# Kernel optimization log

Hardware: AMD Instinct MI355X
Metric: run time of the kernel (lower is better)

## Reference

```python
import jax, jax.numpy as jnp
import numpy as np

B, S, D, H, T = 64, 512, 768, 384, 22  # batch, seq, bert dim, lstm hidden, tagset+2


def setup_inputs() -> dict:
    key = jax.random.key(0)
    ks = jax.random.split(key, 14)
    hidden_states = jax.random.normal(ks[0], (B, S, D), jnp.float32)
    # strictly increasing wordpiece start offsets, -1 padded (per-sample variable length)
    nw = np.array([S // 2 - (b % 16) * 4 for b in range(B)])  # number of valid start ids
    sid = -np.ones((B, S), np.int64)
    msk = np.zeros((B, S), np.int64)
    for b in range(B):
        sid[b, : nw[b]] = 1 + 2 * np.arange(nw[b])  # max = 2*nw-1 <= S-1
        msk[b, : nw[b] + 1] = 1  # word-level mask: nw+1 words incl. CLS slot
    start_ids = jnp.asarray(sid)
    masks = jnp.asarray(msk)
    sc = 0.05
    h0 = jax.random.normal(ks[1], (2, B, H), jnp.float32)
    c0 = jax.random.normal(ks[2], (2, B, H), jnp.float32)
    W_ih_f = jax.random.normal(ks[3], (4 * H, D), jnp.float32) * sc
    W_hh_f = jax.random.normal(ks[4], (4 * H, H), jnp.float32) * sc
    b_ih_f = jax.random.normal(ks[5], (4 * H,), jnp.float32) * sc
    b_hh_f = jax.random.normal(ks[6], (4 * H,), jnp.float32) * sc
    W_ih_b = jax.random.normal(ks[7], (4 * H, D), jnp.float32) * sc
    W_hh_b = jax.random.normal(ks[8], (4 * H, H), jnp.float32) * sc
    b_ih_b = jax.random.normal(ks[9], (4 * H,), jnp.float32) * sc
    b_hh_b = jax.random.normal(ks[10], (4 * H,), jnp.float32) * sc
    W_lin = jax.random.normal(ks[11], (T, 2 * H), jnp.float32) * sc
    b_lin = jax.random.normal(ks[12], (T,), jnp.float32) * sc
    return {"hidden_states": hidden_states, "h0": h0, "c0": c0,
            "W_ih_f": W_ih_f, "W_hh_f": W_hh_f, "b_ih_f": b_ih_f, "b_hh_f": b_hh_f,
            "W_ih_b": W_ih_b, "W_hh_b": W_hh_b, "b_ih_b": b_ih_b, "b_hh_b": b_hh_b,
            "W_lin": W_lin, "b_lin": b_lin, "start_ids": start_ids, "masks": masks}


def _lstm_dir(x, h0, c0, Wih, Whh, bih, bhh, reverse):
    # x: [B,S,D]; torch gate order i,f,g,o
    xg = jnp.einsum('bsd,gd->bsg', x, Wih) + bih + bhh  # [B,S,4H]
    xs = jnp.swapaxes(xg, 0, 1)  # [S,B,4H]
    if reverse:
        xs = xs[::-1]

    def step(carry, xt):
        h, c = carry
        g = xt + h @ Whh.T
        i, f, gg, o = jnp.split(g, 4, axis=-1)
        c = jax.nn.sigmoid(f) * c + jax.nn.sigmoid(i) * jnp.tanh(gg)
        h = jax.nn.sigmoid(o) * jnp.tanh(c)
        return (h, c), h

    _, hs = jax.lax.scan(step, (h0, c0), xs)
    if reverse:
        hs = hs[::-1]
    return jnp.swapaxes(hs, 0, 1)  # [B,S,H]


def _align(hidden_states, start_ids, masks):
    # word t embedding: t==0 -> token 0 (CLS); 1<=t<n -> token start_ids[t]-1
    # (last wordpiece of word t); t==n -> token start_ids[n-1]; else zero-pad.
    Bb, Ss, _ = hidden_states.shape
    t = jnp.arange(Ss)[None, :]
    valid = start_ids >= 0
    n = valid.sum(-1)  # [B] number of valid start ids
    last_sid = jnp.take_along_axis(start_ids, (n - 1)[:, None], axis=1)  # [B,1]
    idx = jnp.where(t == 0, 0,
          jnp.where(t < n[:, None], start_ids - 1,
          jnp.where(t == n[:, None], last_sid, 0)))
    idx = jnp.clip(idx, 0, Ss - 1)
    gathered = jnp.take_along_axis(hidden_states, idx[:, :, None], axis=1)
    sent_len = masks.sum(-1)  # word-level lengths (second loop in torch code)
    keep = (t < sent_len[:, None])[:, :, None]
    return jnp.where(keep, gathered, 0.0)


def reference(hidden_states, h0, c0, W_ih_f, W_hh_f, b_ih_f, b_hh_f,
              W_ih_b, W_hh_b, b_ih_b, b_hh_b, W_lin, b_lin, start_ids, masks):
    embeds = _align(hidden_states, start_ids, masks)  # q=1,k=0 => wordpiece-only
    hf = _lstm_dir(embeds, h0[0], c0[0], W_ih_f, W_hh_f, b_ih_f, b_hh_f, False)
    hb = _lstm_dir(embeds, h0[1], c0[1], W_ih_b, W_hh_b, b_ih_b, b_hh_b, True)
    lstm_out = jnp.concatenate([hf, hb], axis=-1)  # [B,S,2H]
    # dropout1 is identity in eval mode
    feats = lstm_out @ W_lin.T + b_lin  # [B,S,T]
    return feats
```

## Files before the change

kernel.cpp:

```cpp
#include <hip/hip_runtime.h>

typedef unsigned short u16;
typedef unsigned int u32;
typedef unsigned long long u64;

typedef short bf16x8 __attribute__((ext_vector_type(8)));
typedef float f32x4 __attribute__((ext_vector_type(4)));
typedef u32 u32x4 __attribute__((ext_vector_type(4)));

#define NB 64
#define NS 512
#define ND 768
#define NH 384
#define NT_OUT 22
#define S2 272
#define NG 1536
#define MGEMM (NB*S2)
#define MAGIC 0x5A5AA5A5u
#define MAX_RETRY 1000000

__device__ __forceinline__ u16 f2b(float f) {
    u32 u = __float_as_uint(f);
    u32 r = (u + 0x7fffu + ((u >> 16) & 1u)) >> 16;
    return (u16)r;
}
__device__ __forceinline__ float b2f(u16 s) { return __uint_as_float(((u32)s) << 16); }

__device__ __forceinline__ float sigm(float x) {
    return __builtin_amdgcn_rcpf(1.f + __expf(-x));
}
__device__ __forceinline__ float tanh_(float x) {
    return 1.f - 2.f * __builtin_amdgcn_rcpf(1.f + __expf(2.f * x));
}

__device__ __forceinline__ void gl_lds16(const void* g, void* l) {
    __builtin_amdgcn_global_load_lds(
        (const __attribute__((address_space(1))) unsigned int*)g,
        (__attribute__((address_space(3))) unsigned int*)l, 16, 0, 0);
}

__device__ __forceinline__ u32 ld_sc0(const int* p) {
    u32 v;
    asm volatile("global_load_dword %0, %1, off sc0 nt\n\t"
                 "s_waitcnt vmcnt(0)"
                 : "=&v"(v) : "v"(p) : "memory");
    return v;
}
__device__ __forceinline__ void st_sc0(int* p, u32 v) {
    asm volatile("global_store_dword %0, %1, off sc0" :: "v"(p), "v"(v) : "memory");
}

__device__ __forceinline__ void ld6_fast_nw(const u32* p,
        u32x4& A, u32x4& B, u32x4& C, u32x4& D, u32x4& E, u32x4& F) {
    asm volatile(
        "global_load_dwordx4 %0, %6, off sc0 nt\n\t"
        "global_load_dwordx4 %1, %6, off offset:16 sc0 nt\n\t"
        "global_load_dwordx4 %2, %6, off offset:128 sc0 nt\n\t"
        "global_load_dwordx4 %3, %6, off offset:144 sc0 nt\n\t"
        "global_load_dwordx4 %4, %6, off offset:256 sc0 nt\n\t"
        "global_load_dwordx4 %5, %6, off offset:272 sc0 nt"
        : "=&v"(A), "=&v"(B), "=&v"(C), "=&v"(D), "=&v"(E), "=&v"(F)
        : "v"(p) : "memory");
}
__device__ __forceinline__ void ld6_fast_wt(const u32* p,
        u32x4& A, u32x4& B, u32x4& C, u32x4& D, u32x4& E, u32x4& F) {
    asm volatile(
        "global_load_dwordx4 %0, %6, off sc0 nt\n\t"
        "global_load_dwordx4 %1, %6, off offset:16 sc0 nt\n\t"
        "global_load_dwordx4 %2, %6, off offset:128 sc0 nt\n\t"
        "global_load_dwordx4 %3, %6, off offset:144 sc0 nt\n\t"
        "global_load_dwordx4 %4, %6, off offset:256 sc0 nt\n\t"
        "global_load_dwordx4 %5, %6, off offset:272 sc0 nt\n\t"
        "s_waitcnt vmcnt(0)"
        : "=&v"(A), "=&v"(B), "=&v"(C), "=&v"(D), "=&v"(E), "=&v"(F)
        : "v"(p) : "memory");
}
__device__ __forceinline__ void ld6_slow(const u32* p,
        u32x4& A, u32x4& B, u32x4& C, u32x4& D, u32x4& E, u32x4& F) {
    #pragma unroll
    for (int e = 0; e < 4; e++) {
        A[e] = __hip_atomic_load(p + e,      __ATOMIC_RELAXED, __HIP_MEMORY_SCOPE_AGENT);
        B[e] = __hip_atomic_load(p + 4 + e,  __ATOMIC_RELAXED, __HIP_MEMORY_SCOPE_AGENT);
        C[e] = __hip_atomic_load(p + 32 + e, __ATOMIC_RELAXED, __HIP_MEMORY_SCOPE_AGENT);
        D[e] = __hip_atomic_load(p + 36 + e, __ATOMIC_RELAXED, __HIP_MEMORY_SCOPE_AGENT);
        E[e] = __hip_atomic_load(p + 64 + e, __ATOMIC_RELAXED, __HIP_MEMORY_SCOPE_AGENT);
        F[e] = __hip_atomic_load(p + 68 + e, __ATOMIC_RELAXED, __HIP_MEMORY_SCOPE_AGENT);
    }
}
__device__ __forceinline__ void ld6_nw(bool fast, const u32* p,
        u32x4& A, u32x4& B, u32x4& C, u32x4& D, u32x4& E, u32x4& F) {
    if (fast) ld6_fast_nw(p, A, B, C, D, E, F);
    else      ld6_slow(p, A, B, C, D, E, F);
}
__device__ __forceinline__ void ld6_wt(bool fast, const u32* p,
        u32x4& A, u32x4& B, u32x4& C, u32x4& D, u32x4& E, u32x4& F) {
    if (fast) ld6_fast_wt(p, A, B, C, D, E, F);
    else      ld6_slow(p, A, B, C, D, E, F);
}
__device__ __forceinline__ void st8(bool fast, u32* p, u32x4 lo, u32x4 hi) {
    if (fast)
        asm volatile("global_store_dwordx4 %0, %1, off sc0\n\t"
                     "global_store_dwordx4 %0, %2, off offset:16 sc0"
                     :: "v"(p), "v"(lo), "v"(hi) : "memory");
    else {
        #pragma unroll
        for (int e = 0; e < 4; e++) {
            __hip_atomic_store(p + e,     lo[e], __ATOMIC_RELAXED, __HIP_MEMORY_SCOPE_AGENT);
            __hip_atomic_store(p + 4 + e, hi[e], __ATOMIC_RELAXED, __HIP_MEMORY_SCOPE_AGENT);
        }
    }
}
__device__ __forceinline__ void wait_vm6() {
    __builtin_amdgcn_sched_barrier(0);
    asm volatile("s_waitcnt vmcnt(6)" ::: "memory");
    __builtin_amdgcn_sched_barrier(0);
}
__device__ __forceinline__ void wait_vm0() {
    __builtin_amdgcn_sched_barrier(0);
    asm volatile("s_waitcnt vmcnt(0)" ::: "memory");
    __builtin_amdgcn_sched_barrier(0);
}
__device__ __forceinline__ void ldsbar() {
    asm volatile("s_waitcnt lgkmcnt(0)" ::: "memory");
    __builtin_amdgcn_s_barrier();
    __builtin_amdgcn_sched_barrier(0);
}

__device__ __forceinline__ u32 sum6(const u32x4& a, const u32x4& b, const u32x4& c,
                                    const u32x4& d, const u32x4& e, const u32x4& f) {
    u32 s = (a[0] & 0xffffu) + (a[1] & 0xffffu) + (a[2] & 0xffffu) + (a[3] & 0xffffu);
    s += (b[0] & 0xffffu) + (b[1] & 0xffffu) + (b[2] & 0xffffu) + (b[3] & 0xffffu);
    s += (c[0] & 0xffffu) + (c[1] & 0xffffu) + (c[2] & 0xffffu) + (c[3] & 0xffffu);
    s += (d[0] & 0xffffu) + (d[1] & 0xffffu) + (d[2] & 0xffffu) + (d[3] & 0xffffu);
    s += (e[0] & 0xffffu) + (e[1] & 0xffffu) + (e[2] & 0xffffu) + (e[3] & 0xffffu);
    s += (f[0] & 0xffffu) + (f[1] & 0xffffu) + (f[2] & 0xffffu) + (f[3] & 0xffffu);
    return s;
}
__device__ __forceinline__ bf16x8 packf(const u32x4& lo, const u32x4& hi) {
    union { u32 q[4]; bf16x8 v; } U;
    U.q[0] = __builtin_amdgcn_perm(lo[1], lo[0], 0x07060302u);
    U.q[1] = __builtin_amdgcn_perm(lo[3], lo[2], 0x07060302u);
    U.q[2] = __builtin_amdgcn_perm(hi[1], hi[0], 0x07060302u);
    U.q[3] = __builtin_amdgcn_perm(hi[3], hi[2], 0x07060302u);
    return U.v;
}

__global__ void k_prep(const float* __restrict__ hidden, const int* __restrict__ start_ids,
                       const int* __restrict__ masks, u16* __restrict__ embeds) {
    int b = blockIdx.x >> 2;
    int quarter = blockIdx.x & 3;
    int tid = threadIdx.x;
    __shared__ int red[256];
    int cn = 0, cm = 0;
    for (int s = tid; s < NS; s += 256) {
        cn += (start_ids[b * NS + s] >= 0) ? 1 : 0;
        cm += (masks[b * NS + s] != 0) ? 1 : 0;
    }
    red[tid] = cn + (cm << 16);
    __syncthreads();
    #pragma unroll
    for (int off = 128; off > 0; off >>= 1) {
        if (tid < off) red[tid] += red[tid + off];
        __syncthreads();
    }
    int n = red[0] & 0xffff;
    int slen = red[0] >> 16;
    n = min(max(n, 1), NS);
    int last = start_ids[b * NS + n - 1];
    for (int t = quarter * 68; t < quarter * 68 + 68; ++t) {
        int idx;
        if (t == 0) idx = 0;
        else if (t < n) idx = start_ids[b * NS + t] - 1;
        else if (t == n) idx = last;
        else idx = 0;
        idx = min(max(idx, 0), NS - 1);
        bool keep = t < slen;
        const float* src = hidden + ((size_t)b * NS + idx) * ND;
        u16* dst = embeds + ((size_t)b * S2 + t) * ND;
        if (tid < 192) {
            float4 v = keep ? *(const float4*)(src + tid * 4) : make_float4(0.f, 0.f, 0.f, 0.f);
            union { u16 u[4]; uint2 q; } pk;
            pk.u[0] = f2b(v.x); pk.u[1] = f2b(v.y); pk.u[2] = f2b(v.z); pk.u[3] = f2b(v.w);
            *(uint2*)(dst + tid * 4) = pk.q;
        }
    }
}

__global__ void k_weights(const float* __restrict__ wf, const float* __restrict__ wb,
                          const float* __restrict__ bihf, const float* __restrict__ bhhf,
                          const float* __restrict__ bihb, const float* __restrict__ bhhb,
                          const float* __restrict__ h0,
                          u16* __restrict__ wihcat, float* __restrict__ biascat,
                          u16* __restrict__ h0buf) {
    int i0 = blockIdx.x * blockDim.x + threadIdx.x;
    int NTH = gridDim.x * blockDim.x;
    for (size_t i = i0; i < (size_t)2 * NG * ND; i += NTH) {
        size_t nrow = i / ND, k = i - nrow * ND;
        float v = (nrow < NG) ? wf[nrow * ND + k] : wb[(nrow - NG) * ND + k];
        wihcat[i] = f2b(v);
    }
    for (int i = i0; i < 2 * NG; i += NTH)
        biascat[i] = (i < NG) ? bihf[i] + bhhf[i] : bihb[i - NG] + bhhb[i - NG];
    for (int i = i0; i < 2 * NB * NH; i += NTH) h0buf[i] = f2b(h0[i]);
}

__global__ void k_packwhh(const float* __restrict__ whhf, const float* __restrict__ whhb,
                          u16* __restrict__ pack) {
    int ft = blockIdx.x * 256 + threadIdx.x;
    if (ft >= 2 * 4 * 4 * 6 * 12 * 64) return;
    int lane = ft & 63;
    int grp = ft >> 6;
    int ks = grp % 12; grp /= 12;
    int nt = grp % 6;  grp /= 6;
    int w  = grp & 3;  grp >>= 2;
    int qc = grp & 3;
    int d  = grp >> 2;
    const float* W = d ? whhb : whhf;
    int col = w * NH + qc * 96 + nt * 16 + (lane & 15);
    int k0 = ks * 32 + (lane >> 4) * 8;
    u16* dst = pack + (size_t)ft * 8;
    #pragma unroll
    for (int e = 0; e < 8; e++) dst[e] = f2b(W[(size_t)col * NH + k0 + e]);
}

__launch_bounds__(256, 2)
__global__ void k_gemm(const u16* __restrict__ A, const u16* __restrict__ Bw,
                       const float* __restrict__ biascat, u16* __restrict__ xg) {
    __shared__ u16 As[128 * 32];
    __shared__ u16 Bs[128 * 32];
    int tid = threadIdx.x;
    int lane = tid & 63, wid = tid >> 6;
    int l15 = lane & 15, q4 = lane >> 4;
    int bn = blockIdx.x;
    int bm = blockIdx.y;
    int wm = (wid >> 1) * 64, wn = (wid & 1) * 64;
    f32x4 acc[4][4] = {};
    for (int k0 = 0; k0 < ND; k0 += 32) {
        #pragma unroll
        for (int j = 0; j < 2; j++) {
            int fl = tid + j * 256;
            int row = fl >> 2, cb = fl & 3;
            const u16* ga = A + (size_t)(bm * 128 + row) * ND + k0 + cb * 8;
            gl_lds16(ga, &As[(size_t)(wid * 64 + j * 256) * 8]);
            const u16* gb = Bw + (size_t)(bn * 128 + row) * ND + k0 + cb * 8;
            gl_lds16(gb, &Bs[(size_t)(wid * 64 + j * 256) * 8]);
        }
        __syncthreads();
        bf16x8 af[4], bf[4];
        #pragma unroll
        for (int mt = 0; mt < 4; mt++)
            af[mt] = *(const bf16x8*)&As[(wm + mt * 16 + l15) * 32 + q4 * 8];
        #pragma unroll
        for (int nt = 0; nt < 4; nt++)
            bf[nt] = *(const bf16x8*)&Bs[(wn + nt * 16 + l15) * 32 + q4 * 8];
        #pragma unroll
        for (int mt = 0; mt < 4; mt++)
            #pragma unroll
            for (int nt = 0; nt < 4; nt++)
                acc[mt][nt] = __builtin_amdgcn_mfma_f32_16x16x32_bf16(af[mt], bf[nt], acc[mt][nt], 0, 0, 0);
        __syncthreads();
    }
    #pragma unroll
    for (int nt = 0; nt < 4; nt++) {
        int gn = bn * 128 + wn + nt * 16 + l15;
        int d = gn >= NG ? 1 : 0;
        int col = gn - d * NG;
        float bias = biascat[gn];
        #pragma unroll
        for (int mt = 0; mt < 4; mt++) {
            #pragma unroll
            for (int r = 0; r < 4; r++) {
                int m = bm * 128 + wm + mt * 16 + q4 * 4 + r;
                int b = m / S2, t = m - b * S2;
                float v = acc[mt][nt][r] + bias;
                xg[((size_t)(d * NB + b) * S2 + t) * NG + col] = f2b(v);
            }
        }
    }
}

__launch_bounds__(256, 1)
__global__ void k_recur(const u16* __restrict__ whhpack, const u16* __restrict__ xg,
                        const float* __restrict__ biascat, const u16* __restrict__ h0buf,
                        const float* __restrict__ c0, u16* __restrict__ hout,
                        int* __restrict__ flags, u32* __restrict__ xch) {
    const int blk = blockIdx.x;
    const int qc = blk >> 3;
    const int cl = blk & 7;
    const int d = cl >> 2;
    const int g = cl & 3;
    const int tid = threadIdx.x, lane = tid & 63, w = tid >> 6;
    const int q4 = lane >> 4, l15 = lane & 15;

    __shared__ float preact[4][16 * 96];
    __shared__ u16 hlds[16 * 104];
    __shared__ int s_fast;

    bf16x8 bfr[6][12];
    #pragma unroll
    for (int nt = 0; nt < 6; nt++)
        #pragma unroll
        for (int j = 0; j < 12; j++) {
            int ksg = ((qc + (j / 3)) & 3) * 3 + (j % 3);
            bfr[nt][j] = *(const bf16x8*)(whhpack +
                ((size_t)((((d * 4 + qc) * 4 + w) * 6 + nt) * 12 + ksg) * 64 + lane) * 8);
        }

    const int bb = tid / 12;
    const int j0 = (tid % 12) * 8;
    float cre[8];
    if (tid < 192) {
        const float* cp = c0 + (size_t)(d * NB + g * 16 + bb) * NH + qc * 96 + j0;
        #pragma unroll
        for (int e = 0; e < 8; e++) cre[e] = cp[e];
    }
    float biasreg[6];
    #pragma unroll
    for (int nt = 0; nt < 6; nt++)
        biasreg[nt] = biascat[d * NG + w * NH + qc * 96 + nt * 16 + l15];

    if (tid == 0) {
        int* pzb = flags + cl * 64;
        int* pmb = flags + 2048 + cl * 64;
        st_sc0(pzb + qc * 16, MAGIC);
        u32 seen = 1u << qc;
        for (int spin = 0; spin < 512 && seen != 0xFu; ++spin) {
            #pragma unroll
            for (int r = 0; r < 4; ++r)
                if (!((seen >> r) & 1u) && ld_sc0(pzb + r * 16) == MAGIC) seen |= 1u << r;
            __builtin_amdgcn_s_sleep(2);
        }
        __hip_atomic_store(pmb + qc * 16, (int)(0x100u | seen),
                           __ATOMIC_RELAXED, __HIP_MEMORY_SCOPE_AGENT);
        u32 m = 0xFu;
        int spin2 = 0;
        #pragma unroll
        for (int r = 0; r < 4; ++r) {
            u32 v;
            do {
                v = (u32)__hip_atomic_load(pmb + r * 16, __ATOMIC_RELAXED,
                                           __HIP_MEMORY_SCOPE_AGENT);
            } while (!(v & 0x100u) && ++spin2 < MAX_RETRY);
            m &= v;
        }
        s_fast = ((m & 0xFu) == 0xFu && spin2 < MAX_RETRY) ? 1 : 0;
    }
    __syncthreads();
    const bool fast = (s_fast != 0);

    const u16* xgd = xg + (size_t)d * NB * S2 * NG;

    float ci[6][4];
    auto preload = [&](int it2) {
        int s2 = d ? (NS - 1 - it2) : it2;
        if (s2 < S2) {
            const u16* xrow = xgd + ((size_t)(g * 16) * S2 + s2) * NG + w * NH + qc * 96 + l15;
            #pragma unroll
            for (int nt = 0; nt < 6; nt++)
                #pragma unroll
                for (int r = 0; r < 4; r++)
                    ci[nt][r] = b2f(xrow[(size_t)(q4 * 4 + r) * S2 * NG + nt * 16]);
        } else {
            #pragma unroll
            for (int nt = 0; nt < 6; nt++)
                #pragma unroll
                for (int r = 0; r < 4; r++) ci[nt][r] = biasreg[nt];
        }
    };
    preload(0);

    #pragma unroll 1
    for (int it = 0; it < NS; ++it) {
        int s = d ? (NS - 1 - it) : it;
        f32x4 acc[6];

        if (it == 0) {
            bf16x8 af0[12];
            const u16* hp = h0buf + (size_t)(d * NB + g * 16) * NH;
            #pragma unroll
            for (int j = 0; j < 12; j++) {
                int ksg = ((qc + (j / 3)) & 3) * 3 + (j % 3);
                af0[j] = *(const bf16x8*)(hp + (size_t)l15 * NH + ksg * 32 + q4 * 8);
            }
            #pragma unroll
            for (int nt = 0; nt < 6; nt++) {
                acc[nt][0] = ci[nt][0]; acc[nt][1] = ci[nt][1];
                acc[nt][2] = ci[nt][2]; acc[nt][3] = ci[nt][3];
            }
            preload(1);
            #pragma unroll
            for (int j = 0; j < 12; j++)
                #pragma unroll
                for (int nt = 0; nt < 6; nt++)
                    acc[nt] = __builtin_amdgcn_mfma_f32_16x16x32_bf16(af0[j], bfr[nt][j], acc[nt], 0, 0, 0);
        } else {
            bf16x8 afo0 = *(const bf16x8*)&hlds[l15 * 104 + 0 * 32 + q4 * 8];
            bf16x8 afo1 = *(const bf16x8*)&hlds[l15 * 104 + 1 * 32 + q4 * 8];
            bf16x8 afo2 = *(const bf16x8*)&hlds[l15 * 104 + 2 * 32 + q4 * 8];
            const u32 T = (u32)it;
            const u32 want = T * 24u;
            u32* xrow = xch + (((size_t)(T & 3u) * 8 + cl) * 16 + l15) * 384 + q4 * 8;
            u32* pA = xrow + ((qc + 1) & 3) * 96;
            u32* pB = xrow + ((qc + 2) & 3) * 96;
            u32* pC = xrow + ((qc + 3) & 3) * 96;
            u32x4 a0, a1, a2, a3, a4, a5, b0, b1, b2, b3, b4, b5, e0, e1, e2, e3, e4, e5;
            ld6_nw(fast, pA, a0, a1, a2, a3, a4, a5);
            ld6_nw(fast, pB, b0, b1, b2, b3, b4, b5);
            #pragma unroll
            for (int nt = 0; nt < 6; nt++) {
                acc[nt][0] = ci[nt][0]; acc[nt][1] = ci[nt][1];
                acc[nt][2] = ci[nt][2]; acc[nt][3] = ci[nt][3];
            }
            #pragma unroll
            for (int nt = 0; nt < 6; nt++)
                acc[nt] = __builtin_amdgcn_mfma_f32_16x16x32_bf16(afo0, bfr[nt][0], acc[nt], 0, 0, 0);
            #pragma unroll
            for (int nt = 0; nt < 6; nt++)
                acc[nt] = __builtin_amdgcn_mfma_f32_16x16x32_bf16(afo1, bfr[nt][1], acc[nt], 0, 0, 0);
            #pragma unroll
            for (int nt = 0; nt < 6; nt++)
                acc[nt] = __builtin_amdgcn_mfma_f32_16x16x32_bf16(afo2, bfr[nt][2], acc[nt], 0, 0, 0);
            wait_vm6();
            int tries = 0;
            while (!__all(sum6(a0, a1, a2, a3, a4, a5) == want) && ++tries < MAX_RETRY)
                ld6_wt(fast, pA, a0, a1, a2, a3, a4, a5);
            bf16x8 afA0 = packf(a0, a1), afA1 = packf(a2, a3), afA2 = packf(a4, a5);
            ld6_nw(fast, pC, e0, e1, e2, e3, e4, e5);
            #pragma unroll
            for (int nt = 0; nt < 6; nt++)
                acc[nt] = __builtin_amdgcn_mfma_f32_16x16x32_bf16(afA0, bfr[nt][3], acc[nt], 0, 0, 0);
            #pragma unroll
            for (int nt = 0; nt < 6; nt++)
                acc[nt] = __builtin_amdgcn_mfma_f32_16x16x32_bf16(afA1, bfr[nt][4], acc[nt], 0, 0, 0);
            #pragma unroll
            for (int nt = 0; nt < 6; nt++)
                acc[nt] = __builtin_amdgcn_mfma_f32_16x16x32_bf16(afA2, bfr[nt][5], acc[nt], 0, 0, 0);
            wait_vm6();
            tries = 0;
            while (!__all(sum6(b0, b1, b2, b3, b4, b5) == want) && ++tries < MAX_RETRY)
                ld6_wt(fast, pB, b0, b1, b2, b3, b4, b5);
            bf16x8 afB0 = packf(b0, b1), afB1 = packf(b2, b3), afB2 = packf(b4, b5);
            #pragma unroll
            for (int nt = 0; nt < 6; nt++)
                acc[nt] = __builtin_amdgcn_mfma_f32_16x16x32_bf16(afB0, bfr[nt][6], acc[nt], 0, 0, 0);
            #pragma unroll
            for (int nt = 0; nt < 6; nt++)
                acc[nt] = __builtin_amdgcn_mfma_f32_16x16x32_bf16(afB1, bfr[nt][7], acc[nt], 0, 0, 0);
            #pragma unroll
            for (int nt = 0; nt < 6; nt++)
                acc[nt] = __builtin_amdgcn_mfma_f32_16x16x32_bf16(afB2, bfr[nt][8], acc[nt], 0, 0, 0);
            wait_vm0();
            tries = 0;
            while (!__all(sum6(e0, e1, e2, e3, e4, e5) == want) && ++tries < MAX_RETRY)
                ld6_wt(fast, pC, e0, e1, e2, e3, e4, e5);
            bf16x8 afC0 = packf(e0, e1), afC1 = packf(e2, e3), afC2 = packf(e4, e5);
            if (it + 1 < NS) preload(it + 1);
            #pragma unroll
            for (int nt = 0; nt < 6; nt++)
                acc[nt] = __builtin_amdgcn_mfma_f32_16x16x32_bf16(afC0, bfr[nt][9], acc[nt], 0, 0, 0);
            #pragma unroll
            for (int nt = 0; nt < 6; nt++)
                acc[nt] = __builtin_amdgcn_mfma_f32_16x16x32_bf16(afC1, bfr[nt][10], acc[nt], 0, 0, 0);
            #pragma unroll
            for (int nt = 0; nt < 6; nt++)
                acc[nt] = __builtin_amdgcn_mfma_f32_16x16x32_bf16(afC2, bfr[nt][11], acc[nt], 0, 0, 0);
        }

        #pragma unroll
        for (int nt = 0; nt < 6; nt++)
            #pragma unroll
            for (int r = 0; r < 4; r++)
                preact[w][(q4 * 4 + r) * 96 + nt * 16 + l15] = acc[nt][r];
        ldsbar();

        if (tid < 192) {
            int idx = bb * 96 + j0;
            u16* ho = hout + (((size_t)(d * NB + g * 16 + bb)) * NS + s) * NH + qc * 96 + j0;
            union { u16 u[8]; u32x4 v4; } pk;
            #pragma unroll
            for (int e = 0; e < 8; e++) {
                float gi = preact[0][idx + e], gf = preact[1][idx + e];
                float gg = preact[2][idx + e], go = preact[3][idx + e];
                float c = cre[e];
                float cn = sigm(gf) * c + sigm(gi) * tanh_(gg);
                float hn = sigm(go) * tanh_(cn);
                cre[e] = cn;
                pk.u[e] = f2b(hn);
            }
            u32 t2 = (u32)it + 1u;
            u32x4 lo, hi;
            lo[0] = ((u32)pk.u[0] << 16) | t2; lo[1] = ((u32)pk.u[1] << 16) | t2;
            lo[2] = ((u32)pk.u[2] << 16) | t2; lo[3] = ((u32)pk.u[3] << 16) | t2;
            hi[0] = ((u32)pk.u[4] << 16) | t2; hi[1] = ((u32)pk.u[5] << 16) | t2;
            hi[2] = ((u32)pk.u[6] << 16) | t2; hi[3] = ((u32)pk.u[7] << 16) | t2;
            u32* xp = xch + (((size_t)(t2 & 3u) * 8 + cl) * 16 + bb) * 384 + qc * 96 + j0;
            st8(fast, xp, lo, hi);
            *(u32x4*)ho = pk.v4;
            *(u32x4*)&hlds[bb * 104 + j0] = pk.v4;
        }
        wait_vm0();
        ldsbar();
    }
}

__global__ void k_final(const u16* __restrict__ hout, const float* __restrict__ wlin,
                        const float* __restrict__ blin, float* __restrict__ out) {
    int r = blockIdx.x * 256 + threadIdx.x;
    int b = r >> 9, t = r & 511;
    const u16* hf = hout + ((size_t)b * NS + t) * NH;
    const u16* hb = hout + ((size_t)(NB + b) * NS + t) * NH;
    float acc[NT_OUT];
    #pragma unroll
    for (int tt = 0; tt < NT_OUT; tt++) acc[tt] = blin[tt];
    #pragma unroll 1
    for (int half = 0; half < 2; half++) {
        const u16* hp = half ? hb : hf;
        #pragma unroll 1
        for (int k8 = 0; k8 < NH / 8; k8++) {
            uint4 pk = *(const uint4*)(hp + k8 * 8);
            float x[8];
            x[0] = __uint_as_float(pk.x << 16); x[1] = __uint_as_float(pk.x & 0xffff0000u);
            x[2] = __uint_as_float(pk.y << 16); x[3] = __uint_as_float(pk.y & 0xffff0000u);
            x[4] = __uint_as_float(pk.z << 16); x[5] = __uint_as_float(pk.z & 0xffff0000u);
            x[6] = __uint_as_float(pk.w << 16); x[7] = __uint_as_float(pk.w & 0xffff0000u);
            int kk = half * NH + k8 * 8;
            #pragma unroll
            for (int e = 0; e < 8; e++)
                #pragma unroll
                for (int tt = 0; tt < NT_OUT; tt++)
                    acc[tt] += x[e] * wlin[tt * (2 * NH) + kk + e];
        }
    }
    float* op = out + (size_t)r * NT_OUT;
    #pragma unroll
    for (int tt = 0; tt < NT_OUT; tt++) op[tt] = acc[tt];
}

extern "C" void kernel_launch(void* const* d_in, const int* in_sizes, int n_in,
                              void* d_out, int out_size, void* d_ws, size_t ws_size,
                              hipStream_t stream) {
    const float* hidden = (const float*)d_in[0];
    const float* h0     = (const float*)d_in[1];
    const float* c0     = (const float*)d_in[2];
    const float* Wihf   = (const float*)d_in[3];
    const float* Whhf   = (const float*)d_in[4];
    const float* bihf   = (const float*)d_in[5];
    const float* bhhf   = (const float*)d_in[6];
    const float* Wihb   = (const float*)d_in[7];
    const float* Whhb   = (const float*)d_in[8];
    const float* bihb   = (const float*)d_in[9];
    const float* bhhb   = (const float*)d_in[10];
    const float* Wlin   = (const float*)d_in[11];
    const float* blin   = (const float*)d_in[12];
    const int* start_ids = (const int*)d_in[13];
    const int* masks     = (const int*)d_in[14];
    float* out = (float*)d_out;

    char* ws = (char*)d_ws;
    size_t off = 0;
    auto alloc = [&](size_t bytes) { void* p = ws + off; off += (bytes + 255) & ~(size_t)255; return p; };
    u16* embeds   = (u16*)alloc((size_t)MGEMM * ND * 2);
    u16* wihcat   = (u16*)alloc((size_t)2 * NG * ND * 2);
    float* biascat = (float*)alloc((size_t)2 * NG * 4);
    u16* whhpack  = (u16*)alloc((size_t)2 * NG * NH * 2);
    u16* h0buf    = (u16*)alloc((size_t)2 * NB * NH * 2);
    u16* xg       = (u16*)alloc((size_t)2 * NB * S2 * NG * 2);
    u16* hout     = (u16*)alloc((size_t)2 * NB * NS * NH * 2);
    int* flags    = (int*)alloc((size_t)8 * NS * 4);
    u32* xch      = (u32*)alloc((size_t)4 * 8 * 16 * 384 * 4);

    (void)hipMemsetAsync(flags, 0, (size_t)8 * NS * 4, stream);
    (void)hipMemsetAsync(xch, 0, (size_t)4 * 8 * 16 * 384 * 4, stream);
    k_prep<<<256, 256, 0, stream>>>(hidden, start_ids, masks, embeds);
    k_weights<<<512, 256, 0, stream>>>(Wihf, Wihb, bihf, bhhf, bihb, bhhb, h0,
                                       wihcat, biascat, h0buf);
    k_packwhh<<<576, 256, 0, stream>>>(Whhf, Whhb, whhpack);
    dim3 ggrid(2 * NG / 128, MGEMM / 128);
    k_gemm<<<ggrid, 256, 0, stream>>>(embeds, wihcat, biascat, xg);
    k_recur<<<32, 256, 0, stream>>>(whhpack, xg, biascat, h0buf, c0, hout, flags, xch);
    k_final<<<128, 256, 0, stream>>>(hout, Wlin, blin, out);
}
```

Before: 2.657 ms.

## Split LSTM recurrence across six hidden-column chunks per cluster instead of four

Repartitions the recurrent kernel so each cluster of workgroups splits the hidden dimension into 6 chunks of 64 columns rather than 4 chunks of 96. The grid grows from 32 to 48 blocks, and each block does fewer MFMAs per step and now uses all 256 threads for the cell update. The exchange buffer layout, flag handshake and Whh packing are reworked to match. In exchange, every step must poll five peers instead of three, which adds cross-block synchronisation traffic and latency on the critical path.

```diff
diff --git a/kernel.cpp b/kernel.cpp
--- a/kernel.cpp
+++ b/kernel.cpp
@@ -18,6 +18,7 @@
 #define MGEMM (NB*S2)
 #define MAGIC 0x5A5AA5A5u
 #define MAX_RETRY 1000000
+#define NQC 6
 
 __device__ __forceinline__ u16 f2b(float f) {
     u32 u = __float_as_uint(f);
@@ -50,90 +51,71 @@
     asm volatile("global_store_dword %0, %1, off sc0" :: "v"(p), "v"(v) : "memory");
 }
 
-__device__ __forceinline__ void ld6_fast_nw(const u32* p,
-        u32x4& A, u32x4& B, u32x4& C, u32x4& D, u32x4& E, u32x4& F) {
+__device__ __forceinline__ void ld4_fast_nw(const u32* p,
+        u32x4& A, u32x4& B, u32x4& C, u32x4& D) {
     asm volatile(
-        "global_load_dwordx4 %0, %6, off sc0 nt\n\t"
-        "global_load_dwordx4 %1, %6, off offset:16 sc0 nt\n\t"
-        "global_load_dwordx4 %2, %6, off offset:128 sc0 nt\n\t"
-        "global_load_dwordx4 %3, %6, off offset:144 sc0 nt\n\t"
-        "global_load_dwordx4 %4, %6, off offset:256 sc0 nt\n\t"
-        "global_load_dwordx4 %5, %6, off offset:272 sc0 nt"
-        : "=&v"(A), "=&v"(B), "=&v"(C), "=&v"(D), "=&v"(E), "=&v"(F)
+        "global_load_dwordx4 %0, %4, off sc0 nt\n\t"
+        "global_load_dwordx4 %1, %4, off offset:16 sc0 nt\n\t"
+        "global_load_dwordx4 %2, %4, off offset:128 sc0 nt\n\t"
+        "global_load_dwordx4 %3, %4, off offset:144 sc0 nt"
+        : "=&v"(A), "=&v"(B), "=&v"(C), "=&v"(D)
         : "v"(p) : "memory");
 }
-__device__ __forceinline__ void ld6_fast_wt(const u32* p,
-        u32x4& A, u32x4& B, u32x4& C, u32x4& D, u32x4& E, u32x4& F) {
+__device__ __forceinline__ void ld4_fast_wt(const u32* p,
+        u32x4& A, u32x4& B, u32x4& C, u32x4& D) {
     asm volatile(
-        "global_load_dwordx4 %0, %6, off sc0 nt\n\t"
-        "global_load_dwordx4 %1, %6, off offset:16 sc0 nt\n\t"
-        "global_load_dwordx4 %2, %6, off offset:128 sc0 nt\n\t"
-        "global_load_dwordx4 %3, %6, off offset:144 sc0 nt\n\t"
-        "global_load_dwordx4 %4, %6, off offset:256 sc0 nt\n\t"
-        "global_load_dwordx4 %5, %6, off offset:272 sc0 nt\n\t"
+        "global_load_dwordx4 %0, %4, off sc0 nt\n\t"
+        "global_load_dwordx4 %1, %4, off offset:16 sc0 nt\n\t"
+        "global_load_dwordx4 %2, %4, off offset:128 sc0 nt\n\t"
+        "global_load_dwordx4 %3, %4, off offset:144 sc0 nt\n\t"
         "s_waitcnt vmcnt(0)"
-        : "=&v"(A), "=&v"(B), "=&v"(C), "=&v"(D), "=&v"(E), "=&v"(F)
+        : "=&v"(A), "=&v"(B), "=&v"(C), "=&v"(D)
         : "v"(p) : "memory");
 }
-__device__ __forceinline__ void ld6_slow(const u32* p,
-        u32x4& A, u32x4& B, u32x4& C, u32x4& D, u32x4& E, u32x4& F) {
+__device__ __forceinline__ void ld4_slow(const u32* p,
+        u32x4& A, u32x4& B, u32x4& C, u32x4& D) {
     #pragma unroll
     for (int e = 0; e < 4; e++) {
         A[e] = __hip_atomic_load(p + e,      __ATOMIC_RELAXED, __HIP_MEMORY_SCOPE_AGENT);
         B[e] = __hip_atomic_load(p + 4 + e,  __ATOMIC_RELAXED, __HIP_MEMORY_SCOPE_AGENT);
         C[e] = __hip_atomic_load(p + 32 + e, __ATOMIC_RELAXED, __HIP_MEMORY_SCOPE_AGENT);
         D[e] = __hip_atomic_load(p + 36 + e, __ATOMIC_RELAXED, __HIP_MEMORY_SCOPE_AGENT);
-        E[e] = __hip_atomic_load(p + 64 + e, __ATOMIC_RELAXED, __HIP_MEMORY_SCOPE_AGENT);
-        F[e] = __hip_atomic_load(p + 68 + e, __ATOMIC_RELAXED, __HIP_MEMORY_SCOPE_AGENT);
-    }
-}
-__device__ __forceinline__ void ld6_nw(bool fast, const u32* p,
-        u32x4& A, u32x4& B, u32x4& C, u32x4& D, u32x4& E, u32x4& F) {
-    if (fast) ld6_fast_nw(p, A, B, C, D, E, F);
-    else      ld6_slow(p, A, B, C, D, E, F);
-}
-__device__ __forceinline__ void ld6_wt(bool fast, const u32* p,
-        u32x4& A, u32x4& B, u32x4& C, u32x4& D, u32x4& E, u32x4& F) {
-    if (fast) ld6_fast_wt(p, A, B, C, D, E, F);
-    else      ld6_slow(p, A, B, C, D, E, F);
-}
-__device__ __forceinline__ void st8(bool fast, u32* p, u32x4 lo, u32x4 hi) {
+    }
+}
+__device__ __forceinline__ void ld4_nw(bool fast, const u32* p,
+        u32x4& A, u32x4& B, u32x4& C, u32x4& D) {
+    if (fast) ld4_fast_nw(p, A, B, C, D);
+    else      ld4_slow(p, A, B, C, D);
+}
+__device__ __forceinline__ void ld4_wt(bool fast, const u32* p,
+        u32x4& A, u32x4& B, u32x4& C, u32x4& D) {
+    if (fast) ld4_fast_wt(p, A, B, C, D);
+    else      ld4_slow(p, A, B, C, D);
+}
+__device__ __forceinline__ void st4(bool fast, u32* p, u32x4 v) {
     if (fast)
-        asm volatile("global_store_dwordx4 %0, %1, off sc0\n\t"
-                     "global_store_dwordx4 %0, %2, off offset:16 sc0"
-                     :: "v"(p), "v"(lo), "v"(hi) : "memory");
+        asm volatile("global_store_dwordx4 %0, %1, off sc0" :: "v"(p), "v"(v) : "memory");
     else {
         #pragma unroll
-        for (int e = 0; e < 4; e++) {
-            __hip_atomic_store(p + e,     lo[e], __ATOMIC_RELAXED, __HIP_MEMORY_SCOPE_AGENT);
-            __hip_atomic_store(p + 4 + e, hi[e], __ATOMIC_RELAXED, __HIP_MEMORY_SCOPE_AGENT);
-        }
-    }
-}
-__device__ __forceinline__ void wait_vm6() {
-    __builtin_amdgcn_sched_barrier(0);
-    asm volatile("s_waitcnt vmcnt(6)" ::: "memory");
-    __builtin_amdgcn_sched_barrier(0);
-}
-__device__ __forceinline__ void wait_vm0() {
-    __builtin_amdgcn_sched_barrier(0);
-    asm volatile("s_waitcnt vmcnt(0)" ::: "memory");
-    __builtin_amdgcn_sched_barrier(0);
-}
+        for (int e = 0; e < 4; e++)
+            __hip_atomic_store(p + e, v[e], __ATOMIC_RELAXED, __HIP_MEMORY_SCOPE_AGENT);
+    }
+}
+#define WAIT_VM(N) do { __builtin_amdgcn_sched_barrier(0); \
+    asm volatile("s_waitcnt vmcnt(" #N ")" ::: "memory"); \
+    __builtin_amdgcn_sched_barrier(0); } while (0)
 __device__ __forceinline__ void ldsbar() {
     asm volatile("s_waitcnt lgkmcnt(0)" ::: "memory");
     __builtin_amdgcn_s_barrier();
     __builtin_amdgcn_sched_barrier(0);
 }
 
-__device__ __forceinline__ u32 sum6(const u32x4& a, const u32x4& b, const u32x4& c,
-                                    const u32x4& d, const u32x4& e, const u32x4& f) {
+__device__ __forceinline__ u32 sum4(const u32x4& a, const u32x4& b,
+                                    const u32x4& c, const u32x4& d) {
     u32 s = (a[0] & 0xffffu) + (a[1] & 0xffffu) + (a[2] & 0xffffu) + (a[3] & 0xffffu);
     s += (b[0] & 0xffffu) + (b[1] & 0xffffu) + (b[2] & 0xffffu) + (b[3] & 0xffffu);
     s += (c[0] & 0xffffu) + (c[1] & 0xffffu) + (c[2] & 0xffffu) + (c[3] & 0xffffu);
     s += (d[0] & 0xffffu) + (d[1] & 0xffffu) + (d[2] & 0xffffu) + (d[3] & 0xffffu);
-    s += (e[0] & 0xffffu) + (e[1] & 0xffffu) + (e[2] & 0xffffu) + (e[3] & 0xffffu);
-    s += (f[0] & 0xffffu) + (f[1] & 0xffffu) + (f[2] & 0xffffu) + (f[3] & 0xffffu);
     return s;
 }
 __device__ __forceinline__ bf16x8 packf(const u32x4& lo, const u32x4& hi) {
@@ -207,16 +189,16 @@
 __global__ void k_packwhh(const float* __restrict__ whhf, const float* __restrict__ whhb,
                           u16* __restrict__ pack) {
     int ft = blockIdx.x * 256 + threadIdx.x;
-    if (ft >= 2 * 4 * 4 * 6 * 12 * 64) return;
+    if (ft >= 2 * NQC * 4 * 4 * 12 * 64) return;
     int lane = ft & 63;
     int grp = ft >> 6;
     int ks = grp % 12; grp /= 12;
-    int nt = grp % 6;  grp /= 6;
+    int nt = grp & 3;  grp >>= 2;
     int w  = grp & 3;  grp >>= 2;
-    int qc = grp & 3;
-    int d  = grp >> 2;
+    int qc = grp % NQC;
+    int d  = grp / NQC;
     const float* W = d ? whhb : whhf;
-    int col = w * NH + qc * 96 + nt * 16 + (lane & 15);
+    int col = w * NH + qc * 64 + nt * 16 + (lane & 15);
     int k0 = ks * 32 + (lane >> 4) * 8;
     u16* dst = pack + (size_t)ft * 8;
     #pragma unroll
@@ -292,50 +274,50 @@
     const int tid = threadIdx.x, lane = tid & 63, w = tid >> 6;
     const int q4 = lane >> 4, l15 = lane & 15;
 
-    __shared__ float preact[4][16 * 96];
-    __shared__ u16 hlds[16 * 104];
+    __shared__ float preact[4 * 16 * 68];
+    __shared__ u16 hlds[16 * 72];
     __shared__ int s_fast;
 
-    bf16x8 bfr[6][12];
-    #pragma unroll
-    for (int nt = 0; nt < 6; nt++)
+    bf16x8 bfr[4][12];
+    #pragma unroll
+    for (int nt = 0; nt < 4; nt++)
         #pragma unroll
         for (int j = 0; j < 12; j++) {
-            int ksg = ((qc + (j / 3)) & 3) * 3 + (j % 3);
+            int ksg = 2 * ((qc + (j >> 1)) % NQC) + (j & 1);
             bfr[nt][j] = *(const bf16x8*)(whhpack +
-                ((size_t)((((d * 4 + qc) * 4 + w) * 6 + nt) * 12 + ksg) * 64 + lane) * 8);
-        }
-
-    const int bb = tid / 12;
-    const int j0 = (tid % 12) * 8;
-    float cre[8];
-    if (tid < 192) {
-        const float* cp = c0 + (size_t)(d * NB + g * 16 + bb) * NH + qc * 96 + j0;
-        #pragma unroll
-        for (int e = 0; e < 8; e++) cre[e] = cp[e];
-    }
-    float biasreg[6];
-    #pragma unroll
-    for (int nt = 0; nt < 6; nt++)
-        biasreg[nt] = biascat[d * NG + w * NH + qc * 96 + nt * 16 + l15];
+                ((size_t)((((d * NQC + qc) * 4 + w) * 4 + nt) * 12 + ksg) * 64 + lane) * 8);
+        }
+
+    const int bb = tid >> 4;
+    const int jo = (tid & 15) * 4;
+    float cre[4];
+    {
+        const float* cp = c0 + (size_t)(d * NB + g * 16 + bb) * NH + qc * 64 + jo;
+        #pragma unroll
+        for (int e = 0; e < 4; e++) cre[e] = cp[e];
+    }
+    float biasreg[4];
+    #pragma unroll
+    for (int nt = 0; nt < 4; nt++)
+        biasreg[nt] = biascat[d * NG + w * NH + qc * 64 + nt * 16 + l15];
 
     if (tid == 0) {
-        int* pzb = flags + cl * 64;
-        int* pmb = flags + 2048 + cl * 64;
+        int* pzb = flags + cl * 128;
+        int* pmb = flags + 2048 + cl * 128;
         st_sc0(pzb + qc * 16, MAGIC);
         u32 seen = 1u << qc;
-        for (int spin = 0; spin < 512 && seen != 0xFu; ++spin) {
-            #pragma unroll
-            for (int r = 0; r < 4; ++r)
+        for (int spin = 0; spin < 768 && seen != 0x3Fu; ++spin) {
+            #pragma unroll
+            for (int r = 0; r < NQC; ++r)
                 if (!((seen >> r) & 1u) && ld_sc0(pzb + r * 16) == MAGIC) seen |= 1u << r;
             __builtin_amdgcn_s_sleep(2);
         }
         __hip_atomic_store(pmb + qc * 16, (int)(0x100u | seen),
                            __ATOMIC_RELAXED, __HIP_MEMORY_SCOPE_AGENT);
-        u32 m = 0xFu;
+        u32 m = 0x3Fu;
         int spin2 = 0;
         #pragma unroll
-        for (int r = 0; r < 4; ++r) {
+        for (int r = 0; r < NQC; ++r) {
             u32 v;
             do {
                 v = (u32)__hip_atomic_load(pmb + r * 16, __ATOMIC_RELAXED,
@@ -343,26 +325,26 @@
             } while (!(v & 0x100u) && ++spin2 < MAX_RETRY);
             m &= v;
         }
-        s_fast = ((m & 0xFu) == 0xFu && spin2 < MAX_RETRY) ? 1 : 0;
+        s_fast = ((m & 0x3Fu) == 0x3Fu && spin2 < MAX_RETRY) ? 1 : 0;
     }
     __syncthreads();
     const bool fast = (s_fast != 0);
 
     const u16* xgd = xg + (size_t)d * NB * S2 * NG;
 
-    float ci[6][4];
+    float ci[4][4];
     auto preload = [&](int it2) {
         int s2 = d ? (NS - 1 - it2) : it2;
         if (s2 < S2) {
-            const u16* xrow = xgd + ((size_t)(g * 16) * S2 + s2) * NG + w * NH + qc * 96 + l15;
-            #pragma unroll
-            for (int nt = 0; nt < 6; nt++)
+            const u16* xrow = xgd + ((size_t)(g * 16) * S2 + s2) * NG + w * NH + qc * 64 + l15;
+            #pragma unroll
+            for (int nt = 0; nt < 4; nt++)
                 #pragma unroll
                 for (int r = 0; r < 4; r++)
                     ci[nt][r] = b2f(xrow[(size_t)(q4 * 4 + r) * S2 * NG + nt * 16]);
         } else {
             #pragma unroll
-            for (int nt = 0; nt < 6; nt++)
+            for (int nt = 0; nt < 4; nt++)
                 #pragma unroll
                 for (int r = 0; r < 4; r++) ci[nt][r] = biasreg[nt];
         }
@@ -372,18 +354,18 @@
     #pragma unroll 1
     for (int it = 0; it < NS; ++it) {
         int s = d ? (NS - 1 - it) : it;
-        f32x4 acc[6];
+        f32x4 acc[4];
 
         if (it == 0) {
             bf16x8 af0[12];
             const u16* hp = h0buf + (size_t)(d * NB + g * 16) * NH;
             #pragma unroll
             for (int j = 0; j < 12; j++) {
-                int ksg = ((qc + (j / 3)) & 3) * 3 + (j % 3);
+                int ksg = 2 * ((qc + (j >> 1)) % NQC) + (j & 1);
                 af0[j] = *(const bf16x8*)(hp + (size_t)l15 * NH + ksg * 32 + q4 * 8);
             }
             #pragma unroll
-            for (int nt = 0; nt < 6; nt++) {
+            for (int nt = 0; nt < 4; nt++) {
                 acc[nt][0] = ci[nt][0]; acc[nt][1] = ci[nt][1];
                 acc[nt][2] = ci[nt][2]; acc[nt][3] = ci[nt][3];
             }
@@ -391,114 +373,137 @@
             #pragma unroll
             for (int j = 0; j < 12; j++)
                 #pragma unroll
-                for (int nt = 0; nt < 6; nt++)
+                for (int nt = 0; nt < 4; nt++)
                     acc[nt] = __builtin_amdgcn_mfma_f32_16x16x32_bf16(af0[j], bfr[nt][j], acc[nt], 0, 0, 0);
         } else {
-            bf16x8 afo0 = *(const bf16x8*)&hlds[l15 * 104 + 0 * 32 + q4 * 8];
-            bf16x8 afo1 = *(const bf16x8*)&hlds[l15 * 104 + 1 * 32 + q4 * 8];
-            bf16x8 afo2 = *(const bf16x8*)&hlds[l15 * 104 + 2 * 32 + q4 * 8];
             const u32 T = (u32)it;
-            const u32 want = T * 24u;
-            u32* xrow = xch + (((size_t)(T & 3u) * 8 + cl) * 16 + l15) * 384 + q4 * 8;
-            u32* pA = xrow + ((qc + 1) & 3) * 96;
-            u32* pB = xrow + ((qc + 2) & 3) * 96;
-            u32* pC = xrow + ((qc + 3) & 3) * 96;
-            u32x4 a0, a1, a2, a3, a4, a5, b0, b1, b2, b3, b4, b5, e0, e1, e2, e3, e4, e5;
-            ld6_nw(fast, pA, a0, a1, a2, a3, a4, a5);
-            ld6_nw(fast, pB, b0, b1, b2, b3, b4, b5);
-            #pragma unroll
-            for (int nt = 0; nt < 6; nt++) {
+            const u32 want = T * 16u;
+            u32* xb = xch + (size_t)((T & 3u) * 8 + cl) * (NQC * 1024)
+                          + (u32)(l15 * 64 + q4 * 8);
+            u32* p1 = xb + ((qc + 1) % NQC) * 1024;
+            u32* p2 = xb + ((qc + 2) % NQC) * 1024;
+            u32* p3 = xb + ((qc + 3) % NQC) * 1024;
+            u32* p4 = xb + ((qc + 4) % NQC) * 1024;
+            u32* p5 = xb + ((qc + 5) % NQC) * 1024;
+            u32x4 r10, r11, r12, r13, r20, r21, r22, r23, r30, r31, r32, r33;
+            u32x4 r40, r41, r42, r43, r50, r51, r52, r53;
+            ld4_nw(fast, p1, r10, r11, r12, r13);
+            ld4_nw(fast, p2, r20, r21, r22, r23);
+            ld4_nw(fast, p3, r30, r31, r32, r33);
+            ld4_nw(fast, p4, r40, r41, r42, r43);
+            ld4_nw(fast, p5, r50, r51, r52, r53);
+            bf16x8 afo0 = *(const bf16x8*)&hlds[l15 * 72 + q4 * 8];
+            bf16x8 afo1 = *(const bf16x8*)&hlds[l15 * 72 + 32 + q4 * 8];
+            #pragma unroll
+            for (int nt = 0; nt < 4; nt++) {
                 acc[nt][0] = ci[nt][0]; acc[nt][1] = ci[nt][1];
                 acc[nt][2] = ci[nt][2]; acc[nt][3] = ci[nt][3];
             }
             #pragma unroll
-            for (int nt = 0; nt < 6; nt++)
+            for (int nt = 0; nt < 4; nt++)
                 acc[nt] = __builtin_amdgcn_mfma_f32_16x16x32_bf16(afo0, bfr[nt][0], acc[nt], 0, 0, 0);
             #pragma unroll
-            for (int nt = 0; nt < 6; nt++)
+            for (int nt = 0; nt < 4; nt++)
                 acc[nt] = __builtin_amdgcn_mfma_f32_16x16x32_bf16(afo1, bfr[nt][1], acc[nt], 0, 0, 0);
-            #pragma unroll
-            for (int nt = 0; nt < 6; nt++)
-                acc[nt] = __builtin_amdgcn_mfma_f32_16x16x32_bf16(afo2, bfr[nt][2], acc[nt], 0, 0, 0);
-            wait_vm6();
-            int tries = 0;
-            while (!__all(sum6(a0, a1, a2, a3, a4, a5) == want) && ++tries < MAX_RETRY)
-                ld6_wt(fast, pA, a0, a1, a2, a3, a4, a5);
-            bf16x8 afA0 = packf(a0, a1), afA1 = packf(a2, a3), afA2 = packf(a4, a5);
-            ld6_nw(fast, pC, e0, e1, e2, e3, e4, e5);
-            #pragma unroll
-            for (int nt = 0; nt < 6; nt++)
-                acc[nt] = __builtin_amdgcn_mfma_f32_16x16x32_bf16(afA0, bfr[nt][3], acc[nt], 0, 0, 0);
-            #pragma unroll
-            for (int nt = 0; nt < 6; nt++)
-                acc[nt] = __builtin_amdgcn_mfma_f32_16x16x32_bf16(afA1, bfr[nt][4], acc[nt], 0, 0, 0);
-            #pragma unroll
-            for (int nt = 0; nt < 6; nt++)
-                acc[nt] = __builtin_amdgcn_mfma_f32_16x16x32_bf16(afA2, bfr[nt][5], acc[nt], 0, 0, 0);
-            wait_vm6();
+            int tries;
+            WAIT_VM(16);
             tries = 0;
-            while (!__all(sum6(b0, b1, b2, b3, b4, b5) == want) && ++tries < MAX_RETRY)
-                ld6_wt(fast, pB, b0, b1, b2, b3, b4, b5);
-            bf16x8 afB0 = packf(b0, b1), afB1 = packf(b2, b3), afB2 = packf(b4, b5);
-            #pragma unroll
-            for (int nt = 0; nt < 6; nt++)
-                acc[nt] = __builtin_amdgcn_mfma_f32_16x16x32_bf16(afB0, bfr[nt][6], acc[nt], 0, 0, 0);
-            #pragma unroll
-            for (int nt = 0; nt < 6; nt++)
-                acc[nt] = __builtin_amdgcn_mfma_f32_16x16x32_bf16(afB1, bfr[nt][7], acc[nt], 0, 0, 0);
-            #pragma unroll
-            for (int nt = 0; nt < 6; nt++)
-                acc[nt] = __builtin_amdgcn_mfma_f32_16x16x32_bf16(afB2, bfr[nt][8], acc[nt], 0, 0, 0);
-            wait_vm0();
+            while (!__all(sum4(r10, r11, r12, r13) == want) && ++tries < MAX_RETRY)
+                ld4_wt(fast, p1, r10, r11, r12, r13);
+            {
+                bf16x8 lo = packf(r10, r11), hi = packf(r12, r13);
+                #pragma unroll
+                for (int nt = 0; nt < 4; nt++)
+                    acc[nt] = __builtin_amdgcn_mfma_f32_16x16x32_bf16(lo, bfr[nt][2], acc[nt], 0, 0, 0);
+                #pragma unroll
+                for (int nt = 0; nt < 4; nt++)
+                    acc[nt] = __builtin_amdgcn_mfma_f32_16x16x32_bf16(hi, bfr[nt][3], acc[nt], 0, 0, 0);
+            }
+            WAIT_VM(12);
             tries = 0;
-            while (!__all(sum6(e0, e1, e2, e3, e4, e5) == want) && ++tries < MAX_RETRY)
-                ld6_wt(fast, pC, e0, e1, e2, e3, e4, e5);
-            bf16x8 afC0 = packf(e0, e1), afC1 = packf(e2, e3), afC2 = packf(e4, e5);
+            while (!__all(sum4(r20, r21, r22, r23) == want) && ++tries < MAX_RETRY)
+                ld4_wt(fast, p2, r20, r21, r22, r23);
+            {
+                bf16x8 lo = packf(r20, r21), hi = packf(r22, r23);
+                #pragma unroll
+                for (int nt = 0; nt < 4; nt++)
+                    acc[nt] = __builtin_amdgcn_mfma_f32_16x16x32_bf16(lo, bfr[nt][4], acc[nt], 0, 0, 0);
+                #pragma unroll
+                for (int nt = 0; nt < 4; nt++)
+                    acc[nt] = __builtin_amdgcn_mfma_f32_16x16x32_bf16(hi, bfr[nt][5], acc[nt], 0, 0, 0);
+            }
+            WAIT_VM(8);
+            tries = 0;
+            while (!__all(sum4(r30, r31, r32, r33) == want) && ++tries < MAX_RETRY)
+                ld4_wt(fast, p3, r30, r31, r32, r33);
+            {
+                bf16x8 lo = packf(r30, r31), hi = packf(r32, r33);
+                #pragma unroll
+                for (int nt = 0; nt < 4; nt++)
+                    acc[nt] = __builtin_amdgcn_mfma_f32_16x16x32_bf16(lo, bfr[nt][6], acc[nt], 0, 0, 0);
+                #pragma unroll
+                for (int nt = 0; nt < 4; nt++)
+                    acc[nt] = __builtin_amdgcn_mfma_f32_16x16x32_bf16(hi, bfr[nt][7], acc[nt], 0, 0, 0);
+            }
+            WAIT_VM(4);
+            tries = 0;
+            while (!__all(sum4(r40, r41, r42, r43) == want) && ++tries < MAX_RETRY)
+                ld4_wt(fast, p4, r40, r41, r42, r43);
+            {
+                bf16x8 lo = packf(r40, r41), hi = packf(r42, r43);
+                #pragma unroll
+                for (int nt = 0; nt < 4; nt++)
+                    acc[nt] = __builtin_amdgcn_mfma_f32_16x16x32_bf16(lo, bfr[nt][8], acc[nt], 0, 0, 0);
+                #pragma unroll
+                for (int nt = 0; nt < 4; nt++)
+                    acc[nt] = __builtin_amdgcn_mfma_f32_16x16x32_bf16(hi, bfr[nt][9], acc[nt], 0, 0, 0);
+            }
+            WAIT_VM(0);
+            tries = 0;
+            while (!__all(sum4(r50, r51, r52, r53) == want) && ++tries < MAX_RETRY)
+                ld4_wt(fast, p5, r50, r51, r52, r53);
             if (it + 1 < NS) preload(it + 1);
-            #pragma unroll
-            for (int nt = 0; nt < 6; nt++)
-                acc[nt] = __builtin_amdgcn_mfma_f32_16x16x32_bf16(afC0, bfr[nt][9], acc[nt], 0, 0, 0);
-            #pragma unroll
-            for (int nt = 0; nt < 6; nt++)
-                acc[nt] = __builtin_amdgcn_mfma_f32_16x16x32_bf16(afC1, bfr[nt][10], acc[nt], 0, 0, 0);
-            #pragma unroll
-            for (int nt = 0; nt < 6; nt++)
-                acc[nt] = __builtin_amdgcn_mfma_f32_16x16x32_bf16(afC2, bfr[nt][11], acc[nt], 0, 0, 0);
-        }
-
-        #pragma unroll
-        for (int nt = 0; nt < 6; nt++)
+            {
+                bf16x8 lo = packf(r50, r51), hi = packf(r52, r53);
+                #pragma unroll
+                for (int nt = 0; nt < 4; nt++)
+                    acc[nt] = __builtin_amdgcn_mfma_f32_16x16x32_bf16(lo, bfr[nt][10], acc[nt], 0, 0, 0);
+                #pragma unroll
+                for (int nt = 0; nt < 4; nt++)
+                    acc[nt] = __builtin_amdgcn_mfma_f32_16x16x32_bf16(hi, bfr[nt][11], acc[nt], 0, 0, 0);
+            }
+        }
+
+        #pragma unroll
+        for (int nt = 0; nt < 4; nt++)
             #pragma unroll
             for (int r = 0; r < 4; r++)
-                preact[w][(q4 * 4 + r) * 96 + nt * 16 + l15] = acc[nt][r];
+                preact[w * 1088 + (q4 * 4 + r) * 68 + nt * 16 + l15] = acc[nt][r];
         ldsbar();
 
-        if (tid < 192) {
-            int idx = bb * 96 + j0;
-            u16* ho = hout + (((size_t)(d * NB + g * 16 + bb)) * NS + s) * NH + qc * 96 + j0;
-            union { u16 u[8]; u32x4 v4; } pk;
-            #pragma unroll
-            for (int e = 0; e < 8; e++) {
-                float gi = preact[0][idx + e], gf = preact[1][idx + e];
-                float gg = preact[2][idx + e], go = preact[3][idx + e];
+        {
+            int ib = bb * 68 + jo;
+            u16* ho = hout + (((size_t)(d * NB + g * 16 + bb)) * NS + s) * NH + qc * 64 + jo;
+            union { u16 u[4]; uint2 q; } pk;
+            u32x4 tg;
+            u32 t2 = (u32)it + 1u;
+            #pragma unroll
+            for (int e = 0; e < 4; e++) {
+                float gi = preact[0 * 1088 + ib + e], gf = preact[1 * 1088 + ib + e];
+                float gg = preact[2 * 1088 + ib + e], go = preact[3 * 1088 + ib + e];
                 float c = cre[e];
                 float cn = sigm(gf) * c + sigm(gi) * tanh_(gg);
                 float hn = sigm(go) * tanh_(cn);
                 cre[e] = cn;
                 pk.u[e] = f2b(hn);
-            }
-            u32 t2 = (u32)it + 1u;
-            u32x4 lo, hi;
-            lo[0] = ((u32)pk.u[0] << 16) | t2; lo[1] = ((u32)pk.u[1] << 16) | t2;
-            lo[2] = ((u32)pk.u[2] << 16) | t2; lo[3] = ((u32)pk.u[3] << 16) | t2;
-            hi[0] = ((u32)pk.u[4] << 16) | t2; hi[1] = ((u32)pk.u[5] << 16) | t2;
-            hi[2] = ((u32)pk.u[6] << 16) | t2; hi[3] = ((u32)pk.u[7] << 16) | t2;
-            u32* xp = xch + (((size_t)(t2 & 3u) * 8 + cl) * 16 + bb) * 384 + qc * 96 + j0;
-            st8(fast, xp, lo, hi);
-            *(u32x4*)ho = pk.v4;
-            *(u32x4*)&hlds[bb * 104 + j0] = pk.v4;
-        }
-        wait_vm0();
+                tg[e] = ((u32)pk.u[e] << 16) | t2;
+            }
+            u32* xp = xch + (size_t)((t2 & 3u) * 8 + cl) * (NQC * 1024)
+                          + (u32)(qc * 1024 + bb * 64 + jo);
+            st4(fast, xp, tg);
+            *(uint2*)ho = pk.q;
+            *(uint2*)&hlds[bb * 72 + jo] = pk.q;
+        }
         ldsbar();
     }
 }
@@ -567,16 +572,16 @@
     u16* xg       = (u16*)alloc((size_t)2 * NB * S2 * NG * 2);
     u16* hout     = (u16*)alloc((size_t)2 * NB * NS * NH * 2);
     int* flags    = (int*)alloc((size_t)8 * NS * 4);
-    u32* xch      = (u32*)alloc((size_t)4 * 8 * 16 * 384 * 4);
+    u32* xch      = (u32*)alloc((size_t)4 * 8 * NQC * 1024 * 4);
 
     (void)hipMemsetAsync(flags, 0, (size_t)8 * NS * 4, stream);
-    (void)hipMemsetAsync(xch, 0, (size_t)4 * 8 * 16 * 384 * 4, stream);
+    (void)hipMemsetAsync(xch, 0, (size_t)4 * 8 * NQC * 1024 * 4, stream);
     k_prep<<<256, 256, 0, stream>>>(hidden, start_ids, masks, embeds);
     k_weights<<<512, 256, 0, stream>>>(Wihf, Wihb, bihf, bhhf, bihb, bhhb, h0,
                                        wihcat, biascat, h0buf);
     k_packwhh<<<576, 256, 0, stream>>>(Whhf, Whhb, whhpack);
     dim3 ggrid(2 * NG / 128, MGEMM / 128);
     k_gemm<<<ggrid, 256, 0, stream>>>(embeds, wihcat, biascat, xg);
-    k_recur<<<32, 256, 0, stream>>>(whhpack, xg, biascat, h0buf, c0, hout, flags, xch);
+    k_recur<<<48, 256, 0, stream>>>(whhpack, xg, biascat, h0buf, c0, hout, flags, xch);
     k_final<<<128, 256, 0, stream>>>(hout, Wlin, blin, out);
 }
```

Result: slower. 2.770 ms (+4.2%).
